# Performance work log

Measured on AMD Instinct MI355X. Metric: run time of the kernel, lower is better.

The kernel has to match this reference:

```python
import jax, jax.numpy as jnp
import numpy as np

N = 64          # num_nodes (EEG electrodes)
T = 200         # time steps
B = 64          # batch
H = 64          # hidden_dim
K = 3           # cheb_k
F_IN = 1        # input_dim
D_GRU = 2 * H * N  # 8192, GRU input size


def setup_inputs() -> dict:
    key = jax.random.key(0)
    ks = jax.random.split(key, 24)
    s = 0.05
    inp = {
        "x": jax.random.normal(ks[0], (B, N, T), dtype=jnp.float32),
        "spatial_ei": jax.random.randint(ks[1], (2, 512), 0, N, dtype=jnp.int32),
        "spatial_ew": jax.random.uniform(ks[2], (512,), dtype=jnp.float32),
        "functional_ei": jax.random.randint(ks[3], (2, 1024), 0, N, dtype=jnp.int32),
        "functional_ew": jax.random.uniform(ks[4], (1024,), dtype=jnp.float32),
        # ChebConv: K separate Linear(F_IN->H, bias shared once)
        "Wcheb": jax.random.normal(ks[5], (K, F_IN, H), dtype=jnp.float32) * s,
        "bcheb": jnp.zeros((H,), jnp.float32),
        # GCNConv
        "Wgcn": jax.random.normal(ks[6], (F_IN, H), dtype=jnp.float32) * s,
        "bgcn": jnp.zeros((H,), jnp.float32),
        # bidirectional GRU (torch layout: gates r,z,n stacked -> 3H rows)
        "Wih_f": jax.random.normal(ks[7], (3 * H, D_GRU), dtype=jnp.float32) * s,
        "Whh_f": jax.random.normal(ks[8], (3 * H, H), dtype=jnp.float32) * s,
        "bih_f": jnp.zeros((3 * H,), jnp.float32),
        "bhh_f": jnp.zeros((3 * H,), jnp.float32),
        "Wih_b": jax.random.normal(ks[9], (3 * H, D_GRU), dtype=jnp.float32) * s,
        "Whh_b": jax.random.normal(ks[10], (3 * H, H), dtype=jnp.float32) * s,
        "bih_b": jnp.zeros((3 * H,), jnp.float32),
        "bhh_b": jnp.zeros((3 * H,), jnp.float32),
        # attention + classifier heads
        "attn_W": jax.random.normal(ks[11], (2 * H, 1), dtype=jnp.float32) * s,
        "attn_b": jnp.zeros((1,), jnp.float32),
        "clf_W": jax.random.normal(ks[12], (2 * H, 1), dtype=jnp.float32) * s,
        "clf_b": jnp.zeros((1,), jnp.float32),
    }
    return inp


def _gru_scan(xp, Whh, bhh, reverse):
    # xp: [B, T, 3H] precomputed input projection; returns [B, T, H]
    xp_t = jnp.swapaxes(xp, 0, 1)  # [T, B, 3H]
    Hh = Whh.shape[1]

    def step(h, xg):
        hg = h @ Whh.T + bhh
        xr, xz, xn = jnp.split(xg, 3, axis=-1)
        hr, hz, hn = jnp.split(hg, 3, axis=-1)
        r = jax.nn.sigmoid(xr + hr)
        z = jax.nn.sigmoid(xz + hz)
        n = jnp.tanh(xn + r * hn)
        h_new = (1.0 - z) * n + z * h
        return h_new, h_new

    h0 = jnp.zeros((xp.shape[0], Hh), xp.dtype)
    _, hs = jax.lax.scan(step, h0, xp_t, reverse=reverse)
    return jnp.swapaxes(hs, 0, 1)


def _forward(x, spatial_ei, spatial_ew, functional_ei, functional_ew,
             Wcheb, bcheb, Wgcn, bgcn,
             Wih_f, Whh_f, bih_f, bhh_f, Wih_b, Whh_b, bih_b, bhh_b,
             attn_W, attn_b, clf_W, clf_b):
    x = x[..., None]  # [B, N, T, 1] (the x.dim()==3 -> unsqueeze path)
    Bsz, Nn, Tt, _ = x.shape

    # ---- ChebConv (PyG, sym norm, lambda_max=2): L_tilde = -D^-1/2 A D^-1/2
    # (scaled-Laplacian self loops cancel: 2*1/2 - 1 = 0)
    row, col = spatial_ei[0], spatial_ei[1]
    deg = jax.ops.segment_sum(spatial_ew, row, num_segments=Nn)
    dinv = jnp.where(deg > 0, jax.lax.rsqrt(jnp.where(deg > 0, deg, 1.0)), 0.0)
    wn = dinv[row] * spatial_ew * dinv[col]
    # operator S[i, j]: aggregate source j into target i (source_to_target flow)
    S = jnp.zeros((Nn, Nn), x.dtype).at[col, row].add(wn)
    Ltil = -S
    Tx0 = x
    Tx1 = jnp.einsum('ij,bjtf->bitf', Ltil, Tx0)
    out_s = jnp.einsum('bntf,fh->bnth', Tx0, Wcheb[0]) + jnp.einsum('bntf,fh->bnth', Tx1, Wcheb[1])
    for k in range(2, K):
        Tx2 = 2.0 * jnp.einsum('ij,bjtf->bitf', Ltil, Tx1) - Tx0
        out_s = out_s + jnp.einsum('bntf,fh->bnth', Tx2, Wcheb[k])
        Tx0, Tx1 = Tx1, Tx2
    h_sp = out_s + bcheb  # [B, N, T, H]

    # ---- GCNConv (PyG gcn_norm with self loops, weight 1)
    row, col = functional_ei[0], functional_ei[1]
    deg = jax.ops.segment_sum(functional_ew, col, num_segments=Nn) + 1.0
    dinv = jax.lax.rsqrt(deg)
    wn = dinv[row] * functional_ew * dinv[col]
    Sg = jnp.zeros((Nn, Nn), x.dtype).at[col, row].add(wn) + jnp.diag(dinv * dinv)
    h_fn = jnp.einsum('bntf,fh->bnth', jnp.einsum('ij,bjtf->bitf', Sg, x), Wgcn) + bgcn

    # ---- stack over time, flatten nodes
    h = jnp.concatenate([h_sp, h_fn], axis=-1)           # [B, N, T, 2H]
    gru_in = jnp.transpose(h, (0, 2, 1, 3)).reshape(Bsz, Tt, Nn * 2 * H)

    # ---- bidirectional GRU
    xp_f = jnp.einsum('btd,gd->btg', gru_in, Wih_f) + bih_f
    xp_b = jnp.einsum('btd,gd->btg', gru_in, Wih_b) + bih_b
    h_f = _gru_scan(xp_f, Whh_f, bhh_f, reverse=False)
    h_b = _gru_scan(xp_b, Whh_b, bhh_b, reverse=True)
    gru_out = jnp.concatenate([h_f, h_b], axis=-1)       # [B, T, 2H]

    # ---- attention pooling + classifier
    scores = jnp.tanh(gru_out @ attn_W + attn_b)         # [B, T, 1]
    aw = jax.nn.softmax(scores, axis=1)
    ctx = jnp.sum(aw * gru_out, axis=1)                  # [B, 2H]
    return jax.nn.sigmoid(ctx @ clf_W + clf_b)           # [B, 1]


def reference(x, spatial_ei, spatial_ew, functional_ei, functional_ew,
              Wcheb, bcheb, Wgcn, bgcn,
              Wih_f, Whh_f, bih_f, bhh_f, Wih_b, Whh_b, bih_b, bhh_b,
              attn_W, attn_b, clf_W, clf_b):
    return _forward(x, spatial_ei, spatial_ew, functional_ei, functional_ew,
                    Wcheb, bcheb, Wgcn, bgcn,
                    Wih_f, Whh_f, bih_f, bhh_f, Wih_b, Whh_b, bih_b, bhh_b,
                    attn_W, attn_b, clf_W, clf_b)
```

## Files before the change

kernel.cpp:

```cpp
#include <hip/hip_runtime.h>
#include <math.h>

#define Nn 64
#define Tt 200
#define Bb 64

__device__ __forceinline__ float sigm(float x){ return 1.0f/(1.0f+__expf(-x)); }
__device__ __forceinline__ float tanh_fast(float x){
  x = fminf(fmaxf(x, -15.f), 15.f);
  float e = __expf(-2.f*x);
  return (1.f - e)/(1.f + e);
}

typedef __attribute__((ext_vector_type(2))) _Float16 h2v;
typedef __attribute__((ext_vector_type(4))) float f4;

#if __has_builtin(__builtin_amdgcn_fdot2)
#define DOT2(w,hv,acc) __builtin_amdgcn_fdot2((w),(hv),(acc),false)
#else
#define DOT2(w,hv,acc) fmaf((float)(w)[0],(float)(hv)[0], fmaf((float)(w)[1],(float)(hv)[1],(acc)))
#endif

__global__ __launch_bounds__(1024) void k1_graphs(
    const int* __restrict__ sp_ei, const float* __restrict__ sp_ew,
    const int* __restrict__ fn_ei, const float* __restrict__ fn_ew,
    float* __restrict__ Lg, float* __restrict__ L2g, float* __restrict__ Gm)
{
  __shared__ float deg[Nn];
  __shared__ float dinv[Nn];
  __shared__ float S[64*68];
  const int tid = threadIdx.x;

  if (tid < Nn) deg[tid] = 0.f;
  for (int i=tid;i<64*68;i+=1024) S[i]=0.f;
  __syncthreads();
  if (tid < 512) atomicAdd(&deg[sp_ei[tid]], sp_ew[tid]);
  __syncthreads();
  if (tid < Nn) dinv[tid] = (deg[tid] > 0.f) ? rsqrtf(deg[tid]) : 0.f;
  __syncthreads();
  if (tid < 512) {
    int r = sp_ei[tid], c = sp_ei[512+tid];
    atomicAdd(&S[c*68 + r], dinv[r]*sp_ew[tid]*dinv[c]);
  }
  __syncthreads();
  for (int i=tid;i<4096;i+=1024) Lg[i] = -S[(i>>6)*68 + (i&63)];
  {
    const int n = tid>>4, mb = (tid&15)*4;
    float a0=0.f,a1=0.f,a2=0.f,a3=0.f;
    for (int j=0;j<64;j++){
      float snj = S[n*68+j];
      float4 v = *(const float4*)&S[j*68+mb];
      a0=fmaf(snj,v.x,a0); a1=fmaf(snj,v.y,a1);
      a2=fmaf(snj,v.z,a2); a3=fmaf(snj,v.w,a3);
    }
    L2g[n*64+mb+0] = 2.f*a0 - (n==mb+0 ? 1.f : 0.f);
    L2g[n*64+mb+1] = 2.f*a1 - (n==mb+1 ? 1.f : 0.f);
    L2g[n*64+mb+2] = 2.f*a2 - (n==mb+2 ? 1.f : 0.f);
    L2g[n*64+mb+3] = 2.f*a3 - (n==mb+3 ? 1.f : 0.f);
  }
  __syncthreads();

  if (tid < Nn) deg[tid] = 0.f;
  for (int i=tid;i<64*68;i+=1024) S[i]=0.f;
  __syncthreads();
  atomicAdd(&deg[fn_ei[1024+tid]], fn_ew[tid]);
  __syncthreads();
  if (tid < Nn) dinv[tid] = rsqrtf(deg[tid] + 1.f);
  __syncthreads();
  {
    int r = fn_ei[tid], c = fn_ei[1024+tid];
    atomicAdd(&S[c*68 + r], dinv[r]*fn_ew[tid]*dinv[c]);
  }
  __syncthreads();
  if (tid < Nn) S[tid*68 + tid] += dinv[tid]*dinv[tid];
  __syncthreads();
  for (int i=tid;i<4096;i+=1024) Gm[i] = S[(i>>6)*68 + (i&63)];
}

__global__ __launch_bounds__(64) void k2_aeff(
    const float* __restrict__ Wih_f, const float* __restrict__ bih_f,
    const float* __restrict__ Wih_b, const float* __restrict__ bih_b,
    const float* __restrict__ Wcheb, const float* __restrict__ bcheb,
    const float* __restrict__ Wgcn,  const float* __restrict__ bgcn,
    const float* __restrict__ Lg, const float* __restrict__ L2g,
    const float* __restrict__ Gm,
    float* __restrict__ Aeff, float* __restrict__ constv)
{
  const int g = blockIdx.x;
  const int dir = (g >= 192) ? 1 : 0;
  const int grow = dir ? g - 192 : g;
  const float* Wih = dir ? Wih_b : Wih_f;
  const float* bih = dir ? bih_b : bih_f;

  __shared__ float wrow[64*129];
  __shared__ float arow[256];
  const int tid = threadIdx.x;

  const float4* W4 = (const float4*)(Wih + (size_t)grow*8192);
  for (int i4 = tid; i4 < 2048; i4 += 64) {
    float4 v = W4[i4];
    int base = i4*4, row = base>>7, col = base&127;
    float* dst = &wrow[row*129+col];
    dst[0]=v.x; dst[1]=v.y; dst[2]=v.z; dst[3]=v.w;
  }
  __syncthreads();

  const int n = tid;
  float a0=0.f,a1=0.f,a2=0.f,a3=0.f,cp=0.f;
  for (int c=0;c<64;c++) {
    float w1 = wrow[n*129 + c];
    a0 = fmaf(w1, Wcheb[c],     a0);
    a1 = fmaf(w1, Wcheb[64+c],  a1);
    a2 = fmaf(w1, Wcheb[128+c], a2);
    cp = fmaf(w1, bcheb[c],     cp);
    float w2 = wrow[n*129 + 64 + c];
    a3 = fmaf(w2, Wgcn[c], a3);
    cp = fmaf(w2, bgcn[c], cp);
  }
  arow[n*4+0]=a0; arow[n*4+1]=a1; arow[n*4+2]=a2; arow[n*4+3]=a3;
  for (int off=32; off; off>>=1) cp += __shfl_down(cp, off, 64);
  if (tid==0) constv[g] = cp + bih[grow];
  __syncthreads();

  const int m = tid;
  float ae = arow[m*4+0];
  for (int nn2=0; nn2<64; nn2++) {
    ae = fmaf(arow[nn2*4+1], Lg [nn2*64+m], ae);
    ae = fmaf(arow[nn2*4+2], L2g[nn2*64+m], ae);
    ae = fmaf(arow[nn2*4+3], Gm [nn2*64+m], ae);
  }
  Aeff[g*64+m] = ae;
}

__global__ __launch_bounds__(256) void k4_gemm(
    const float* __restrict__ x, const float* __restrict__ Aeff,
    const float* __restrict__ constv, float* __restrict__ xp)
{
  const int m0 = blockIdx.x*64, g0 = blockIdx.y*64;
  __shared__ float sX[64*68];
  __shared__ float sA[64*68];
  const int tid = threadIdx.x;

  {
    const int row = tid & 63;
    const int kq  = tid >> 6;
    const int m = m0 + row;
    const int b = m / 200;
    const int t = m - b*200;
    const float* xb = x + (size_t)b*64*200 + t;
    #pragma unroll
    for (int kk=0; kk<16; ++kk) {
      int k = kq*16 + kk;
      sX[k*68 + row] = xb[(size_t)k*200];
    }
  }
  {
    const float4* A4 = (const float4*)Aeff;
    #pragma unroll
    for (int i=0;i<4;i++) {
      int f = tid + i*256;
      int r2 = f >> 4, kq2 = f & 15;
      float4 w = A4[(g0+r2)*16 + kq2];
      sA[(kq2*4+0)*68 + r2] = w.x;
      sA[(kq2*4+1)*68 + r2] = w.y;
      sA[(kq2*4+2)*68 + r2] = w.z;
      sA[(kq2*4+3)*68 + r2] = w.w;
    }
  }
  __syncthreads();

  const int tm = tid & 15, tn = tid >> 4;
  float acc[4][4] = {};
  #pragma unroll 8
  for (int k=0;k<64;k++) {
    float4 a  = *(const float4*)&sX[k*68 + tm*4];
    float4 bb = *(const float4*)&sA[k*68 + tn*4];
    float av[4]={a.x,a.y,a.z,a.w}, bv[4]={bb.x,bb.y,bb.z,bb.w};
    #pragma unroll
    for (int i=0;i<4;i++)
      #pragma unroll
      for (int j=0;j<4;j++)
        acc[i][j] = fmaf(av[i], bv[j], acc[i][j]);
  }

  float cv[4];
  #pragma unroll
  for (int j=0;j<4;j++) cv[j] = constv[g0 + tn*4 + j];
  #pragma unroll
  for (int i=0;i<4;i++) {
    int mrow = m0 + tm*4 + i;
    #pragma unroll
    for (int j=0;j<4;j++)
      xp[mrow*384 + g0 + tn*4 + j] = acc[i][j] + cv[j];
  }
}

__global__ __launch_bounds__(64)
__attribute__((amdgpu_waves_per_eu(1, 1)))
void k5_gru(
    const float* __restrict__ xp,
    const float* __restrict__ Whh_f, const float* __restrict__ bhh_f,
    const float* __restrict__ Whh_b, const float* __restrict__ bhh_b,
    float* __restrict__ gru_out)
{
  const int bd = blockIdx.x;
  const int b = bd >> 1, dir = bd & 1;
  const int g = threadIdx.x & 63;
  const float* Whh = dir ? Whh_b : Whh_f;
  const float* bhh = dir ? bhh_b : bhh_f;

  h2v wr[32], wz[32], wn[32];
  #pragma unroll
  for (int i=0;i<32;i++){
    float2 a = ((const float2*)(Whh + (size_t)g*64))[i];
    float2 bq= ((const float2*)(Whh + (size_t)(64+g)*64))[i];
    float2 c = ((const float2*)(Whh + (size_t)(128+g)*64))[i];
    wr[i] = h2v{(_Float16)a.x, (_Float16)a.y};
    wz[i] = h2v{(_Float16)bq.x,(_Float16)bq.y};
    wn[i] = h2v{(_Float16)c.x, (_Float16)c.y};
  }
  const float br_ = bhh[g], bz_ = bhh[64+g], bn_ = bhh[128+g];

  __shared__ __align__(16) _Float16 hsh[64];
  hsh[g] = (_Float16)0.f;

  const int t0 = dir ? (Tt-1) : 0;
  const int tstep = dir ? -1 : 1;
  const float* xb = xp + (size_t)(b*Tt)*384 + dir*192 + g;
  float* gout = gru_out + (size_t)(b*Tt)*128 + dir*64 + g;

  float h = 0.f;
  float xrA = xb[(size_t)t0*384], xzA = xb[(size_t)t0*384+64], xnA = xb[(size_t)t0*384+128];
  const int t1 = t0 + tstep;
  float xrB = xb[(size_t)t1*384], xzB = xb[(size_t)t1*384+64], xnB = xb[(size_t)t1*384+128];

  int t = t0;
  auto STEP = [&](float& xr, float& xz, float& xn){
    h2v hv[32];
    {
      const uint4* hp4 = (const uint4*)hsh;
      #pragma unroll
      for (int q=0;q<8;q++){
        union { uint4 v; h2v p[4]; } uu;
        uu.v = hp4[q];
        hv[q*4+0]=uu.p[0]; hv[q*4+1]=uu.p[1]; hv[q*4+2]=uu.p[2]; hv[q*4+3]=uu.p[3];
      }
    }

    const float cxr = xr, cxz = xz, cxn = xn;
    const int tpre = t + 2*tstep;
    if ((unsigned)tpre < (unsigned)Tt) {
      xr = xb[(size_t)tpre*384];
      xz = xb[(size_t)tpre*384+64];
      xn = xb[(size_t)tpre*384+128];
    }

    float ar0=0.f,ar1=0.f,az0=0.f,az1=0.f,an0=0.f,an1=0.f;
    #pragma unroll
    for (int i=0;i<32;i+=2){
      ar0 = DOT2(wr[i],  hv[i],  ar0);  az0 = DOT2(wz[i],  hv[i],  az0);  an0 = DOT2(wn[i],  hv[i],  an0);
      ar1 = DOT2(wr[i+1],hv[i+1],ar1);  az1 = DOT2(wz[i+1],hv[i+1],az1);  an1 = DOT2(wn[i+1],hv[i+1],an1);
    }

    float r   = sigm(cxr + (ar0+ar1) + br_);
    float z   = sigm(cxz + (az0+az1) + bz_);
    float nn2 = tanh_fast(cxn + r*((an0+an1) + bn_));
    float hnew = (1.f - z)*nn2 + z*h;
    h = hnew;
    hsh[g] = (_Float16)hnew;
    gout[(size_t)t*128] = hnew;
    t += tstep;
  };

  for (int sp=0; sp<Tt; sp+=2) { STEP(xrA,xzA,xnA); STEP(xrB,xzB,xnB); }
}

__global__ __launch_bounds__(256) void k6_attn(
    const float* __restrict__ gru_out,
    const float* __restrict__ attn_W, const float* __restrict__ attn_b,
    const float* __restrict__ clf_W,  const float* __restrict__ clf_b,
    float* __restrict__ out)
{
  const int b = blockIdx.x, tid = threadIdx.x;
  const int wv = tid >> 6, ln = tid & 63;
  __shared__ float aW[128], cW[128];
  __shared__ float s_s[Tt];
  __shared__ float wred[4];
  __shared__ float part[2][128];
  if (tid < 128) { aW[tid]=attn_W[tid]; cW[tid]=clf_W[tid]; }
  __syncthreads();

  float sc = -1e30f;
  if (tid < Tt) {
    const float* row = gru_out + (size_t)(b*Tt + tid)*128;
    float acc = 0.f;
    for (int j=0;j<128;j++) acc = fmaf(row[j], aW[j], acc);
    sc = tanhf(acc + attn_b[0]);
    s_s[tid] = sc;
  }
  float m = sc;
  #pragma unroll
  for (int off=32; off; off>>=1) m = fmaxf(m, __shfl_xor(m, off, 64));
  if (ln==0) wred[wv] = m;
  __syncthreads();
  const float mx = fmaxf(fmaxf(wred[0],wred[1]), fmaxf(wred[2],wred[3]));

  float e = 0.f;
  if (tid < Tt) { e = __expf(sc - mx); s_s[tid] = e; }
  float s = e;
  #pragma unroll
  for (int off=32; off; off>>=1) s += __shfl_xor(s, off, 64);
  __syncthreads();
  if (ln==0) wred[wv] = s;
  __syncthreads();
  const float total = wred[0]+wred[1]+wred[2]+wred[3];

  const int j = tid & 127, half = tid >> 7;
  float c = 0.f;
  const float* gb = gru_out + (size_t)(b*Tt)*128 + j;
  for (int t = half*100; t < half*100 + 100; ++t)
    c = fmaf(s_s[t], gb[(size_t)t*128], c);
  part[half][j] = c;
  __syncthreads();

  float p = 0.f;
  if (tid < 128) p = ((part[0][j] + part[1][j]) / total) * cW[j];
  #pragma unroll
  for (int off=32; off; off>>=1) p += __shfl_xor(p, off, 64);
  __syncthreads();
  if (ln==0) wred[wv] = p;
  __syncthreads();
  if (tid==0) out[b] = sigm(wred[0] + wred[1] + clf_b[0]);
}

extern "C" void kernel_launch(void* const* d_in, const int* in_sizes, int n_in,
                              void* d_out, int out_size, void* d_ws, size_t ws_size,
                              hipStream_t stream)
{
  const float* x      = (const float*)d_in[0];
  const int*   sp_ei  = (const int*)  d_in[1];
  const float* sp_ew  = (const float*)d_in[2];
  const int*   fn_ei  = (const int*)  d_in[3];
  const float* fn_ew  = (const float*)d_in[4];
  const float* Wcheb  = (const float*)d_in[5];
  const float* bcheb  = (const float*)d_in[6];
  const float* Wgcn   = (const float*)d_in[7];
  const float* bgcn   = (const float*)d_in[8];
  const float* Wih_f  = (const float*)d_in[9];
  const float* Whh_f  = (const float*)d_in[10];
  const float* bih_f  = (const float*)d_in[11];
  const float* bhh_f  = (const float*)d_in[12];
  const float* Wih_b  = (const float*)d_in[13];
  const float* Whh_b  = (const float*)d_in[14];
  const float* bih_b  = (const float*)d_in[15];
  const float* bhh_b  = (const float*)d_in[16];
  const float* attn_W = (const float*)d_in[17];
  const float* attn_b = (const float*)d_in[18];
  const float* clf_W  = (const float*)d_in[19];
  const float* clf_b  = (const float*)d_in[20];
  float* out = (float*)d_out;

  float* ws     = (float*)d_ws;
  float* Lg     = ws;
  float* L2g    = Lg   + 4096;
  float* Gm     = L2g  + 4096;
  float* Aeff   = Gm   + 4096;
  float* constv = Aeff + 24576;
  float* xp     = constv + 512;
  float* gro    = xp   + 4915200;

  hipLaunchKernelGGL(k1_graphs,    dim3(1),      dim3(1024), 0, stream,
                     sp_ei, sp_ew, fn_ei, fn_ew, Lg, L2g, Gm);
  hipLaunchKernelGGL(k2_aeff,      dim3(384),    dim3(64),   0, stream,
                     Wih_f, bih_f, Wih_b, bih_b, Wcheb, bcheb, Wgcn, bgcn,
                     Lg, L2g, Gm, Aeff, constv);
  hipLaunchKernelGGL(k4_gemm,      dim3(200, 6), dim3(256),  0, stream,
                     x, Aeff, constv, xp);
  hipLaunchKernelGGL(k5_gru,       dim3(128),    dim3(64),   0, stream,
                     xp, Whh_f, bhh_f, Whh_b, bhh_b, gro);
  hipLaunchKernelGGL(k6_attn,      dim3(64),     dim3(256),  0, stream,
                     gro, attn_W, attn_b, clf_W, clf_b, out);
}
```

Measured before the change: 132.1 us.

## Store GRU input projections and outputs in fp16, enlarge GEMM row tile

The xp projection buffer and gru_out are now stored as fp16 instead of fp32, which halves the global memory traffic between the GEMM, the GRU recurrence and the attention kernel. The GEMM tile grows from 64 to 128 rows per block, with 8x4 outputs per thread and packed 8-byte fp16 stores. The GRU loads fp16 ushorts and converts them to float. The cost is reduced precision in the stored intermediates and more registers per GEMM thread.

Measured after the change: 132.4 us. Within noise of the previous version (+0.2%).

```diff
diff --git a/kernel.cpp b/kernel.cpp
--- a/kernel.cpp
+++ b/kernel.cpp
@@ -20,6 +20,10 @@
 #else
 #define DOT2(w,hv,acc) fmaf((float)(w)[0],(float)(hv)[0], fmaf((float)(w)[1],(float)(hv)[1],(acc)))
 #endif
+
+__device__ __forceinline__ float h2f(ushort u){
+  return (float)__builtin_bit_cast(_Float16, u);
+}
 
 __global__ __launch_bounds__(1024) void k1_graphs(
     const int* __restrict__ sp_ei, const float* __restrict__ sp_ew,
@@ -134,24 +138,24 @@
 
 __global__ __launch_bounds__(256) void k4_gemm(
     const float* __restrict__ x, const float* __restrict__ Aeff,
-    const float* __restrict__ constv, float* __restrict__ xp)
-{
-  const int m0 = blockIdx.x*64, g0 = blockIdx.y*64;
-  __shared__ float sX[64*68];
+    const float* __restrict__ constv, _Float16* __restrict__ xp)
+{
+  const int m0 = blockIdx.x*128, g0 = blockIdx.y*64;
+  __shared__ float sX[64*132];
   __shared__ float sA[64*68];
   const int tid = threadIdx.x;
 
   {
-    const int row = tid & 63;
-    const int kq  = tid >> 6;
+    const int row = tid & 127;
+    const int kq  = tid >> 7;
     const int m = m0 + row;
     const int b = m / 200;
     const int t = m - b*200;
     const float* xb = x + (size_t)b*64*200 + t;
     #pragma unroll
-    for (int kk=0; kk<16; ++kk) {
-      int k = kq*16 + kk;
-      sX[k*68 + row] = xb[(size_t)k*200];
+    for (int kk=0; kk<32; ++kk) {
+      int k = kq*32 + kk;
+      sX[k*132 + row] = xb[(size_t)k*200];
     }
   }
   {
@@ -170,14 +174,17 @@
   __syncthreads();
 
   const int tm = tid & 15, tn = tid >> 4;
-  float acc[4][4] = {};
-  #pragma unroll 8
+  float acc[8][4] = {};
+  #pragma unroll 4
   for (int k=0;k<64;k++) {
-    float4 a  = *(const float4*)&sX[k*68 + tm*4];
+    const float* xr = &sX[k*132 + tm*8];
+    float4 a0 = *(const float4*)xr;
+    float4 a1 = *(const float4*)(xr+4);
     float4 bb = *(const float4*)&sA[k*68 + tn*4];
-    float av[4]={a.x,a.y,a.z,a.w}, bv[4]={bb.x,bb.y,bb.z,bb.w};
-    #pragma unroll
-    for (int i=0;i<4;i++)
+    float av[8]={a0.x,a0.y,a0.z,a0.w,a1.x,a1.y,a1.z,a1.w};
+    float bv[4]={bb.x,bb.y,bb.z,bb.w};
+    #pragma unroll
+    for (int i=0;i<8;i++)
       #pragma unroll
       for (int j=0;j<4;j++)
         acc[i][j] = fmaf(av[i], bv[j], acc[i][j]);
@@ -187,21 +194,23 @@
   #pragma unroll
   for (int j=0;j<4;j++) cv[j] = constv[g0 + tn*4 + j];
   #pragma unroll
-  for (int i=0;i<4;i++) {
-    int mrow = m0 + tm*4 + i;
+  for (int i=0;i<8;i++) {
+    int mrow = m0 + tm*8 + i;
+    union { ushort u[4]; uint2 v; } pk;
     #pragma unroll
     for (int j=0;j<4;j++)
-      xp[mrow*384 + g0 + tn*4 + j] = acc[i][j] + cv[j];
+      pk.u[j] = __builtin_bit_cast(ushort, (_Float16)(acc[i][j] + cv[j]));
+    *(uint2*)&xp[(size_t)mrow*384 + g0 + tn*4] = pk.v;
   }
 }
 
 __global__ __launch_bounds__(64)
 __attribute__((amdgpu_waves_per_eu(1, 1)))
 void k5_gru(
-    const float* __restrict__ xp,
+    const _Float16* __restrict__ xp,
     const float* __restrict__ Whh_f, const float* __restrict__ bhh_f,
     const float* __restrict__ Whh_b, const float* __restrict__ bhh_b,
-    float* __restrict__ gru_out)
+    _Float16* __restrict__ gru_out)
 {
   const int bd = blockIdx.x;
   const int b = bd >> 1, dir = bd & 1;
@@ -226,16 +235,16 @@
 
   const int t0 = dir ? (Tt-1) : 0;
   const int tstep = dir ? -1 : 1;
-  const float* xb = xp + (size_t)(b*Tt)*384 + dir*192 + g;
-  float* gout = gru_out + (size_t)(b*Tt)*128 + dir*64 + g;
+  const ushort* xb = (const ushort*)xp + (size_t)(b*Tt)*384 + dir*192 + g;
+  _Float16* gout = gru_out + (size_t)(b*Tt)*128 + dir*64 + g;
 
   float h = 0.f;
-  float xrA = xb[(size_t)t0*384], xzA = xb[(size_t)t0*384+64], xnA = xb[(size_t)t0*384+128];
+  ushort xrA = xb[(size_t)t0*384], xzA = xb[(size_t)t0*384+64], xnA = xb[(size_t)t0*384+128];
   const int t1 = t0 + tstep;
-  float xrB = xb[(size_t)t1*384], xzB = xb[(size_t)t1*384+64], xnB = xb[(size_t)t1*384+128];
+  ushort xrB = xb[(size_t)t1*384], xzB = xb[(size_t)t1*384+64], xnB = xb[(size_t)t1*384+128];
 
   int t = t0;
-  auto STEP = [&](float& xr, float& xz, float& xn){
+  auto STEP = [&](ushort& xr, ushort& xz, ushort& xn){
     h2v hv[32];
     {
       const uint4* hp4 = (const uint4*)hsh;
@@ -247,7 +256,7 @@
       }
     }
 
-    const float cxr = xr, cxz = xz, cxn = xn;
+    const float cxr = h2f(xr), cxz = h2f(xz), cxn = h2f(xn);
     const int tpre = t + 2*tstep;
     if ((unsigned)tpre < (unsigned)Tt) {
       xr = xb[(size_t)tpre*384];
@@ -267,8 +276,9 @@
     float nn2 = tanh_fast(cxn + r*((an0+an1) + bn_));
     float hnew = (1.f - z)*nn2 + z*h;
     h = hnew;
-    hsh[g] = (_Float16)hnew;
-    gout[(size_t)t*128] = hnew;
+    _Float16 hf = (_Float16)hnew;
+    hsh[g] = hf;
+    gout[(size_t)t*128] = hf;
     t += tstep;
   };
 
@@ -276,7 +286,7 @@
 }
 
 __global__ __launch_bounds__(256) void k6_attn(
-    const float* __restrict__ gru_out,
+    const _Float16* __restrict__ gru_out,
     const float* __restrict__ attn_W, const float* __restrict__ attn_b,
     const float* __restrict__ clf_W,  const float* __restrict__ clf_b,
     float* __restrict__ out)
@@ -292,9 +302,9 @@
 
   float sc = -1e30f;
   if (tid < Tt) {
-    const float* row = gru_out + (size_t)(b*Tt + tid)*128;
+    const _Float16* row = gru_out + (size_t)(b*Tt + tid)*128;
     float acc = 0.f;
-    for (int j=0;j<128;j++) acc = fmaf(row[j], aW[j], acc);
+    for (int j=0;j<128;j++) acc = fmaf((float)row[j], aW[j], acc);
     sc = tanhf(acc + attn_b[0]);
     s_s[tid] = sc;
   }
@@ -317,9 +327,9 @@
 
   const int j = tid & 127, half = tid >> 7;
   float c = 0.f;
-  const float* gb = gru_out + (size_t)(b*Tt)*128 + j;
+  const _Float16* gb = gru_out + (size_t)(b*Tt)*128 + j;
   for (int t = half*100; t < half*100 + 100; ++t)
-    c = fmaf(s_s[t], gb[(size_t)t*128], c);
+    c = fmaf(s_s[t], (float)gb[(size_t)t*128], c);
   part[half][j] = c;
   __syncthreads();
 
@@ -366,15 +376,15 @@
   float* Gm     = L2g  + 4096;
   float* Aeff   = Gm   + 4096;
   float* constv = Aeff + 24576;
-  float* xp     = constv + 512;
-  float* gro    = xp   + 4915200;
+  _Float16* xp  = (_Float16*)(constv + 512);
+  _Float16* gro = (_Float16*)(constv + 512 + 2457600);
 
   hipLaunchKernelGGL(k1_graphs,    dim3(1),      dim3(1024), 0, stream,
                      sp_ei, sp_ew, fn_ei, fn_ew, Lg, L2g, Gm);
   hipLaunchKernelGGL(k2_aeff,      dim3(384),    dim3(64),   0, stream,
                      Wih_f, bih_f, Wih_b, bih_b, Wcheb, bcheb, Wgcn, bgcn,
                      Lg, L2g, Gm, Aeff, constv);
-  hipLaunchKernelGGL(k4_gemm,      dim3(200, 6), dim3(256),  0, stream,
+  hipLaunchKernelGGL(k4_gemm,      dim3(100, 6), dim3(256),  0, stream,
                      x, Aeff, constv, xp);
   hipLaunchKernelGGL(k5_gru,       dim3(128),    dim3(64),   0, stream,
                      xp, Whh_f, bhh_f, Whh_b, bhh_b, gro);
```
